# Kernel tuning notes

Measured on AMD Instinct MI355X. Metric: run time of the kernel, lower is better.

## Reference

```python
import jax, jax.numpy as jnp
import numpy as np

EPS_DIV = 1e-6    # safe_div clamp
EPS_NORM = 1e-12  # F.normalize eps
EPS_PD = 1e-6     # F.pairwise_distance eps (added to the difference)


def setup_inputs() -> dict:
    key = jax.random.key(0)
    k1, k2, k3 = jax.random.split(key, 3)
    B, N, D, C = 8, 2048, 512, 8192
    x = jax.random.normal(k1, (B, N, D), dtype=jnp.float32)
    W = jax.random.normal(k2, (D, D), dtype=jnp.float32) * (1.0 / np.sqrt(D))
    codebook = jax.random.normal(k3, (C, D), dtype=jnp.float32)
    return {"x": x, "W": W, "codebook": codebook}


def reference(x, W, codebook):
    sg = jax.lax.stop_gradient
    # implicit codebook = Linear(dim, dim, bias=False)(codebook)  -> codebook @ W^T
    imp = codebook @ W.T                                  # [C, D]

    lead = x.shape[:-1]
    D = x.shape[-1]
    xf = x.reshape(-1, D)                                 # [T, D]

    # nearest-neighbor search (no_grad in original): squared-dist argmin == cdist argmin
    d2 = (jnp.sum(xf * xf, axis=-1, keepdims=True)
          - 2.0 * (xf @ imp.T)
          + jnp.sum(imp * imp, axis=-1)[None, :])         # [T, C]
    indices = jnp.argmin(sg(d2), axis=-1)                 # [T]

    qf = imp[indices]                                     # [T, D] gather

    # commit loss: (pairwise_distance(x, q.detach())**2).mean(); torch adds eps to the diff
    diff = xf - sg(qf) + EPS_PD
    commit_loss = jnp.mean(jnp.sum(diff * diff, axis=-1))

    # rotation trick
    norm_x = jnp.linalg.norm(xf, axis=-1, keepdims=True)  # [T, 1]
    norm_q = jnp.linalg.norm(qf, axis=-1, keepdims=True)
    u = xf / jnp.maximum(norm_x, EPS_DIV)
    q = qf / jnp.maximum(norm_q, EPS_DIV)
    s = u + q
    w = sg(s / jnp.maximum(jnp.linalg.norm(s, axis=-1, keepdims=True), EPS_NORM))
    e = xf
    # e - 2 (e.w) w + 2 (e.u_sg) q_sg   (rank-1 products per row)
    rot = (e
           - 2.0 * jnp.sum(e * w, axis=-1, keepdims=True) * w
           + 2.0 * jnp.sum(e * sg(u), axis=-1, keepdims=True) * sg(q))
    quantized = rot * sg(norm_q / jnp.maximum(norm_x, EPS_DIV))

    quantized = quantized.reshape(*lead, D)
    indices = indices.reshape(*lead)
    return quantized, indices, commit_loss
```

## Files before the change

### kernel.cpp

```cpp
#include <hip/hip_runtime.h>
#include <cstdint>
#include <cstddef>

#define DD 512
#define TT 16384
#define CC 8192
#define SPLITC 64
#define EPS_DIV 1e-6f
#define EPS_NORM 1e-12f
#define EPS_PD 1e-6f

typedef _Float16 half8 __attribute__((ext_vector_type(8)));
typedef _Float16 half4 __attribute__((ext_vector_type(4)));
typedef float floatx4 __attribute__((ext_vector_type(4)));

#define GLDS16(g, l) __builtin_amdgcn_global_load_lds( \
    (const __attribute__((address_space(1))) void*)(g), \
    (__attribute__((address_space(3))) void*)(l), 16, 0, 0)

__global__ __launch_bounds__(128) void k_split(const float* __restrict__ src,
                                               _Float16* __restrict__ dst) {
  const int row = blockIdx.x;
  const int col = threadIdx.x * 4;
  float4 v = *(const float4*)(src + (size_t)row * DD + col);
  half4 h, l;
  h.x = (_Float16)v.x; l.x = (_Float16)(v.x - (float)h.x);
  h.y = (_Float16)v.y; l.y = (_Float16)(v.y - (float)h.y);
  h.z = (_Float16)v.z; l.z = (_Float16)(v.z - (float)h.z);
  h.w = (_Float16)v.w; l.w = (_Float16)(v.w - (float)h.w);
  *(half4*)(dst + (size_t)row * 1024 + col) = h;
  *(half4*)(dst + (size_t)row * 1024 + 512 + col) = l;
}

__global__ __launch_bounds__(128) void k_cast16(const float* __restrict__ src,
                                                _Float16* __restrict__ dst) {
  const int row = blockIdx.x;
  const int col = threadIdx.x * 4;
  float4 v = *(const float4*)(src + (size_t)row * DD + col);
  half4 h;
  h.x = (_Float16)v.x; h.y = (_Float16)v.y;
  h.z = (_Float16)v.z; h.w = (_Float16)v.w;
  *(half4*)(dst + (size_t)row * DD + col) = h;
}

__global__ __launch_bounds__(256) void k_gemm_mfma(
    const _Float16* __restrict__ cbs, const _Float16* __restrict__ Ws,
    float* __restrict__ imp, _Float16* __restrict__ ih) {
  __shared__ __align__(16) char smem[65536];
  const int tid = threadIdx.x;
  const int w = tid >> 6, lane = tid & 63;
  const int quad = lane >> 4, l15 = lane & 15;
  const int wm = (w & 1) * 64, wn = (w >> 1) * 64;
  const int c0 = blockIdx.x * 128;
  const int n0 = blockIdx.y * 128;

  const int srow8 = lane >> 3;
  const int scol = ((lane & 7) ^ srow8) << 3;
  size_t arow[4], brow[4];
#pragma unroll
  for (int j = 0; j < 4; ++j) {
    arow[j] = (size_t)(c0 + j * 32 + w * 8 + srow8) * 1024 + scol;
    brow[j] = (size_t)(n0 + j * 32 + w * 8 + srow8) * 1024 + scol;
  }
  int aoff[4], boff[4];
#pragma unroll
  for (int i = 0; i < 4; ++i) {
    aoff[i] = ((wm + i * 16 + l15) * 64 + ((quad ^ (l15 & 7)) << 3)) * 2;
    boff[i] = ((wn + i * 16 + l15) * 64 + ((quad ^ (l15 & 7)) << 3)) * 2;
  }

  auto stage = [&](int buf, int ak, int bk) {
    char* ab = smem + buf * 32768;
    char* bb = ab + 16384;
#pragma unroll
    for (int j = 0; j < 4; ++j) {
      GLDS16(cbs + arow[j] + ak, (_Float16*)ab + (j * 32 + w * 8) * 64);
      GLDS16(Ws  + brow[j] + bk, (_Float16*)bb + (j * 32 + w * 8) * 64);
    }
  };

  floatx4 acc[4][4] = {};
  stage(0, 0, 0);
#pragma unroll 2
  for (int it = 0; it < 24; ++it) {
    __syncthreads();
    if (it < 23) {
      const int n = it + 1;
      const int p = n >> 3, kk = n & 7;
      const int ak = ((p == 2) ? 512 : 0) + kk * 64;
      const int bk = ((p == 1) ? 512 : 0) + kk * 64;
      stage(n & 1, ak, bk);
    }
    const char* ab = smem + (it & 1) * 32768;
    const char* bb = ab + 16384;
#pragma unroll
    for (int ks = 0; ks < 2; ++ks) {
      const int kx = ks * 64;
      half8 a[4], b[4];
#pragma unroll
      for (int mi = 0; mi < 4; ++mi)
        a[mi] = *(const half8*)(ab + (aoff[mi] ^ kx));
#pragma unroll
      for (int ni = 0; ni < 4; ++ni)
        b[ni] = *(const half8*)(bb + (boff[ni] ^ kx));
#pragma unroll
      for (int mi = 0; mi < 4; ++mi)
#pragma unroll
        for (int ni = 0; ni < 4; ++ni)
          acc[mi][ni] = __builtin_amdgcn_mfma_f32_16x16x32_f16(
              a[mi], b[ni], acc[mi][ni], 0, 0, 0);
    }
  }
#pragma unroll
  for (int mi = 0; mi < 4; ++mi)
#pragma unroll
    for (int r = 0; r < 4; ++r) {
      const int c = c0 + wm + mi * 16 + quad * 4 + r;
#pragma unroll
      for (int ni = 0; ni < 4; ++ni) {
        const int d = n0 + wn + ni * 16 + l15;
        const float v = acc[mi][ni][r];
        imp[(size_t)c * DD + d] = v;
        ih[(size_t)c * DD + d] = (_Float16)v;
      }
    }
}

__global__ __launch_bounds__(256) void k_row_norm2(
    const float* __restrict__ imp, float* __restrict__ cnorm) {
  const int lane = threadIdx.x & 63;
  const int row = blockIdx.x * 4 + (threadIdx.x >> 6);
  const float* p = imp + (size_t)row * DD + lane * 8;
  float4 a = *(const float4*)p;
  float4 b = *(const float4*)(p + 4);
  float s = a.x * a.x + a.y * a.y + a.z * a.z + a.w * a.w +
            b.x * b.x + b.y * b.y + b.z * b.z + b.w * b.w;
#pragma unroll
  for (int m = 1; m < 64; m <<= 1) s += __shfl_xor(s, m);
  if (lane == 0) cnorm[row] = s;
}

__global__ __launch_bounds__(256) void k_dist_top2(
    const _Float16* __restrict__ xh, const _Float16* __restrict__ ih,
    const float* __restrict__ cnorm,
    float* __restrict__ bval, int* __restrict__ bidx) {
  __shared__ __align__(16) char smem[65536];
  const int tid = threadIdx.x;
  const int w = tid >> 6, lane = tid & 63;
  const int quad = lane >> 4, l15 = lane & 15;
  const int wm = (w & 1) * 64, wn = (w >> 1) * 64;
  const int r0 = blockIdx.x * 128;
  const int c0 = blockIdx.y * 128;

  const int srow8 = lane >> 3;
  const int scol = ((lane & 7) ^ srow8) << 3;
  size_t arow[4], brow[4];
#pragma unroll
  for (int j = 0; j < 4; ++j) {
    arow[j] = (size_t)(r0 + j * 32 + w * 8 + srow8) * DD + scol;
    brow[j] = (size_t)(c0 + j * 32 + w * 8 + srow8) * DD + scol;
  }
  int aoff[4], boff[4];
#pragma unroll
  for (int i = 0; i < 4; ++i) {
    aoff[i] = ((wm + i * 16 + l15) * 64 + ((quad ^ (l15 & 7)) << 3)) * 2;
    boff[i] = ((wn + i * 16 + l15) * 64 + ((quad ^ (l15 & 7)) << 3)) * 2;
  }

  auto stage = [&](int buf, int k0) {
    char* ab = smem + buf * 32768;
    char* bb = ab + 16384;
#pragma unroll
    for (int j = 0; j < 4; ++j) {
      GLDS16(xh + arow[j] + k0, (_Float16*)ab + (j * 32 + w * 8) * 64);
      GLDS16(ih + brow[j] + k0, (_Float16*)bb + (j * 32 + w * 8) * 64);
    }
  };

  floatx4 acc[4][4] = {};
  stage(0, 0);
#pragma unroll
  for (int kk = 0; kk < 8; ++kk) {
    __syncthreads();
    if (kk < 7) stage((kk + 1) & 1, (kk + 1) * 64);
    const char* ab = smem + (kk & 1) * 32768;
    const char* bb = ab + 16384;
#pragma unroll
    for (int ks = 0; ks < 2; ++ks) {
      const int kx = ks * 64;
      half8 a[4], b[4];
#pragma unroll
      for (int mi = 0; mi < 4; ++mi)
        a[mi] = *(const half8*)(ab + (aoff[mi] ^ kx));
#pragma unroll
      for (int ni = 0; ni < 4; ++ni)
        b[ni] = *(const half8*)(bb + (boff[ni] ^ kx));
#pragma unroll
      for (int mi = 0; mi < 4; ++mi)
#pragma unroll
        for (int ni = 0; ni < 4; ++ni)
          acc[mi][ni] = __builtin_amdgcn_mfma_f32_16x16x32_f16(
              a[mi], b[ni], acc[mi][ni], 0, 0, 0);
    }
  }
  float best[16];
  int bsti[16];
#pragma unroll
  for (int mi = 0; mi < 4; ++mi)
#pragma unroll
    for (int r = 0; r < 4; ++r) {
      const int s = mi * 4 + r;
      best[s] = 3.4e38f; bsti[s] = 0;
#pragma unroll
      for (int ni = 0; ni < 4; ++ni) {
        const int c = c0 + wn + ni * 16 + l15;
        const float v = fmaf(-2.0f, acc[mi][ni][r], cnorm[c]);
        if (v < best[s]) { best[s] = v; bsti[s] = c; }
      }
    }
  __syncthreads();
  float* rv = (float*)smem;
  int* ri = (int*)(smem + 16896);
  const int e = (w >> 1) * 16 + l15;
#pragma unroll
  for (int mi = 0; mi < 4; ++mi)
#pragma unroll
    for (int r = 0; r < 4; ++r) {
      const int row = wm + mi * 16 + quad * 4 + r;
      rv[row * 33 + e] = best[mi * 4 + r];
      ri[row * 33 + e] = bsti[mi * 4 + r];
    }
  __syncthreads();
  if (tid < 128) {
    float v1 = 3.4e38f, v2 = 3.4e38f;
    int i1 = 0x7fffffff, i2 = 0x7fffffff;
#pragma unroll
    for (int t = 0; t < 32; ++t) {
      const float v = rv[tid * 33 + t];
      const int i = ri[tid * 33 + t];
      if (v < v1 || (v == v1 && i < i1)) {
        v2 = v1; i2 = i1; v1 = v; i1 = i;
      } else if (v < v2 || (v == v2 && i < i2)) {
        v2 = v; i2 = i;
      }
    }
    const size_t o = ((size_t)blockIdx.y * TT + r0 + tid) * 2;
    bval[o] = v1; bval[o + 1] = v2;
    bidx[o] = i1; bidx[o + 1] = i2;
  }
}

__global__ __launch_bounds__(256) void k_epilogue(
    const float* __restrict__ x, const float* __restrict__ imp,
    const float* __restrict__ cnorm,
    const float* __restrict__ bval, const int* __restrict__ bidx,
    float* __restrict__ outq, float* __restrict__ outidx,
    float* __restrict__ rloss) {
  const int lane = threadIdx.x & 63;
  const int row = blockIdx.x * 4 + (threadIdx.x >> 6);
  const size_t o = ((size_t)lane * TT + row) * 2;
  float v1 = bval[o], v2 = bval[o + 1];
  int i1 = bidx[o], i2 = bidx[o + 1];
#pragma unroll
  for (int m = 1; m < 64; m <<= 1) {
    const float w1 = __shfl_xor(v1, m), w2 = __shfl_xor(v2, m);
    const int j1 = __shfl_xor(i1, m), j2 = __shfl_xor(i2, m);
    if (w1 < v1 || (w1 == v1 && j1 < i1)) {
      if (v1 < w2 || (v1 == w2 && i1 < j2)) { v2 = v1; i2 = i1; }
      else { v2 = w2; i2 = j2; }
      v1 = w1; i1 = j1;
    } else {
      if (w1 < v2 || (w1 == v2 && j1 < i2)) { v2 = w1; i2 = j1; }
    }
  }
  const float* xr = x + (size_t)row * DD + lane * 8;
  float e[8], qa[8], qb[8];
  *(float4*)&e[0] = *(const float4*)xr;
  *(float4*)&e[4] = *(const float4*)(xr + 4);
  const float* q1p = imp + (size_t)i1 * DD + lane * 8;
  const float* q2p = imp + (size_t)i2 * DD + lane * 8;
  *(float4*)&qa[0] = *(const float4*)q1p;
  *(float4*)&qa[4] = *(const float4*)(q1p + 4);
  *(float4*)&qb[0] = *(const float4*)q2p;
  *(float4*)&qb[4] = *(const float4*)(q2p + 4);
  float d1 = 0.f, d2 = 0.f;
#pragma unroll
  for (int k = 0; k < 8; ++k) {
    d1 = fmaf(e[k], qa[k], d1);
    d2 = fmaf(e[k], qb[k], d2);
  }
#pragma unroll
  for (int m = 1; m < 64; m <<= 1) {
    d1 += __shfl_xor(d1, m);
    d2 += __shfl_xor(d2, m);
  }
  const float s1 = fmaf(-2.0f, d1, cnorm[i1]);
  const float s2 = fmaf(-2.0f, d2, cnorm[i2]);
  const bool use2 = (s2 < s1) || (s2 == s1 && i2 < i1);
  const int idx = use2 ? i2 : i1;
  float q[8];
#pragma unroll
  for (int k = 0; k < 8; ++k) q[k] = use2 ? qb[k] : qa[k];

  float xx = 0.f, qq = 0.f, xq = 0.f, cl = 0.f;
#pragma unroll
  for (int k = 0; k < 8; ++k) {
    xx = fmaf(e[k], e[k], xx);
    qq = fmaf(q[k], q[k], qq);
    xq = fmaf(e[k], q[k], xq);
    float d = e[k] - q[k] + EPS_PD;
    cl = fmaf(d, d, cl);
  }
#pragma unroll
  for (int m = 1; m < 64; m <<= 1) {
    xx += __shfl_xor(xx, m);
    qq += __shfl_xor(qq, m);
    xq += __shfl_xor(xq, m);
    cl += __shfl_xor(cl, m);
  }
  const float nx = sqrtf(xx), nq = sqrtf(qq);
  const float dx = fmaxf(nx, EPS_DIV), dq = fmaxf(nq, EPS_DIV);
  const float uu = xx / (dx * dx);
  const float qq2 = qq / (dq * dq);
  const float uq = xq / (dx * dq);
  const float ss = uu + qq2 + 2.0f * uq;
  const float dn = fmaxf(sqrtf(ss), EPS_NORM);
  const float es = xx / dx + xq / dq;
  const float a = 2.0f * es / (dn * dn);
  const float b = 2.0f * (xx / dx);
  const float scale = nq / dx;

  float ov[8];
#pragma unroll
  for (int k = 0; k < 8; ++k) {
    const float qp = q[k] / dq;
    const float sk = e[k] / dx + qp;
    ov[k] = (e[k] - a * sk + b * qp) * scale;
  }
  float* op = outq + (size_t)row * DD + lane * 8;
  *(float4*)op = *(const float4*)&ov[0];
  *(float4*)(op + 4) = *(const float4*)&ov[4];
  if (lane == 0) {
    outidx[row] = (float)idx;
    rloss[row] = cl;
  }
}

__global__ __launch_bounds__(256) void k_loss_final(
    const float* __restrict__ rloss, float* __restrict__ out) {
  __shared__ double red[256];
  const int tid = threadIdx.x;
  double s = 0.0;
  for (int i = tid; i < TT; i += 256) s += (double)rloss[i];
  red[tid] = s;
  __syncthreads();
  for (int st = 128; st > 0; st >>= 1) {
    if (tid < st) red[tid] += red[tid + st];
    __syncthreads();
  }
  if (tid == 0) out[0] = (float)(red[0] / (double)TT);
}

extern "C" void kernel_launch(void* const* d_in, const int* in_sizes, int n_in,
                              void* d_out, int out_size, void* d_ws, size_t ws_size,
                              hipStream_t stream) {
  const float* x  = (const float*)d_in[0];
  const float* W  = (const float*)d_in[1];
  const float* cb = (const float*)d_in[2];
  float* out = (float*)d_out;

  float* imp = (float*)d_ws;
  _Float16* ih = (_Float16*)(imp + (size_t)CC * DD);
  _Float16* cbs = ih + (size_t)CC * DD;
  _Float16* xh = cbs;
  _Float16* Ws = cbs + (size_t)CC * 1024;
  float* cnorm = (float*)(Ws + (size_t)DD * 1024);
  float* bval  = cnorm + CC;
  int*   bidx  = (int*)(bval + (size_t)SPLITC * TT * 2);
  float* rloss = (float*)(bidx + (size_t)SPLITC * TT * 2);

  float* out_q    = out;
  float* out_idx  = out + (size_t)TT * DD;
  float* out_loss = out_idx + TT;

  k_split<<<CC, 128, 0, stream>>>(cb, cbs);
  k_split<<<DD, 128, 0, stream>>>(W, Ws);
  k_gemm_mfma<<<dim3(CC / 128, DD / 128), 256, 0, stream>>>(cbs, Ws, imp, ih);
  k_row_norm2<<<CC / 4, 256, 0, stream>>>(imp, cnorm);
  k_cast16<<<TT, 128, 0, stream>>>(x, xh);
  k_dist_top2<<<dim3(TT / 128, SPLITC), 256, 0, stream>>>(xh, ih, cnorm, bval, bidx);
  k_epilogue<<<TT / 4, 256, 0, stream>>>(x, imp, cnorm, bval, bidx, out_q, out_idx, rloss);
  k_loss_final<<<1, 256, 0, stream>>>(rloss, out_loss);
}
```

Before: 353.5 us.

## Loop over codebook tiles per block, fuse prep kernels, stage GEMM stores

The distance kernel now has each block sweep four 128-wide codebook tiles with a running argmin. The split across codebook chunks drops from 64 to 16, so the partial top-2 buffer and the epilogue merge shrink. The K tile goes from 64 to 32 with a smaller LDS footprint, which may raise occupancy. Separate prep launches are fused into combined kernels (codebook/W split, x cast plus codebook norms), and the codebook GEMM writes its output through LDS for coalesced stores. Fewer blocks and a longer serial loop per block trade parallelism for less reduction traffic.

Measured after the change: 422.9 us. 1.2x slower.

```diff
diff --git a/kernel.cpp b/kernel.cpp
--- a/kernel.cpp
+++ b/kernel.cpp
@@ -5,7 +5,7 @@
 #define DD 512
 #define TT 16384
 #define CC 8192
-#define SPLITC 64
+#define SPLITC 16
 #define EPS_DIV 1e-6f
 #define EPS_NORM 1e-12f
 #define EPS_PD 1e-6f
@@ -18,10 +18,21 @@
     (const __attribute__((address_space(1))) void*)(g), \
     (__attribute__((address_space(3))) void*)(l), 16, 0, 0)
 
-__global__ __launch_bounds__(128) void k_split(const float* __restrict__ src,
-                                               _Float16* __restrict__ dst) {
-  const int row = blockIdx.x;
-  const int col = threadIdx.x * 4;
+__global__ __launch_bounds__(256) void k_prep(
+    const float* __restrict__ cb, const float* __restrict__ W,
+    _Float16* __restrict__ cbs, _Float16* __restrict__ Ws) {
+  const int b = blockIdx.x;
+  const float* src;
+  _Float16* dst;
+  int row;
+  if (b < CC / 2) {
+    row = b * 2 + (threadIdx.x >> 7);
+    src = cb; dst = cbs;
+  } else {
+    row = (b - CC / 2) * 2 + (threadIdx.x >> 7);
+    src = W; dst = Ws;
+  }
+  const int col = (threadIdx.x & 127) * 4;
   float4 v = *(const float4*)(src + (size_t)row * DD + col);
   half4 h, l;
   h.x = (_Float16)v.x; l.x = (_Float16)(v.x - (float)h.x);
@@ -30,17 +41,6 @@
   h.w = (_Float16)v.w; l.w = (_Float16)(v.w - (float)h.w);
   *(half4*)(dst + (size_t)row * 1024 + col) = h;
   *(half4*)(dst + (size_t)row * 1024 + 512 + col) = l;
-}
-
-__global__ __launch_bounds__(128) void k_cast16(const float* __restrict__ src,
-                                                _Float16* __restrict__ dst) {
-  const int row = blockIdx.x;
-  const int col = threadIdx.x * 4;
-  float4 v = *(const float4*)(src + (size_t)row * DD + col);
-  half4 h;
-  h.x = (_Float16)v.x; h.y = (_Float16)v.y;
-  h.z = (_Float16)v.z; h.w = (_Float16)v.w;
-  *(half4*)(dst + (size_t)row * DD + col) = h;
 }
 
 __global__ __launch_bounds__(256) void k_gemm_mfma(
@@ -111,90 +111,126 @@
               a[mi], b[ni], acc[mi][ni], 0, 0, 0);
     }
   }
+  __syncthreads();
+  float* Csh = (float*)smem;
 #pragma unroll
   for (int mi = 0; mi < 4; ++mi)
 #pragma unroll
     for (int r = 0; r < 4; ++r) {
-      const int c = c0 + wm + mi * 16 + quad * 4 + r;
+      const int row = wm + mi * 16 + quad * 4 + r;
+      const int key = (row & 7) << 2;
 #pragma unroll
       for (int ni = 0; ni < 4; ++ni) {
-        const int d = n0 + wn + ni * 16 + l15;
-        const float v = acc[mi][ni][r];
-        imp[(size_t)c * DD + d] = v;
-        ih[(size_t)c * DD + d] = (_Float16)v;
+        const int col = wn + ni * 16 + l15;
+        Csh[row * 128 + (col ^ key)] = acc[mi][ni][r];
       }
     }
-}
-
-__global__ __launch_bounds__(256) void k_row_norm2(
+  __syncthreads();
+#pragma unroll
+  for (int i = 0; i < 16; ++i) {
+    const int row = (tid >> 5) * 16 + i;
+    const int col = (tid & 31) * 4;
+    const int key = (row & 7) << 2;
+    const float4 v = *(const float4*)&Csh[row * 128 + (col ^ key)];
+    *(float4*)&imp[(size_t)(c0 + row) * DD + n0 + col] = v;
+    half4 h;
+    h.x = (_Float16)v.x; h.y = (_Float16)v.y;
+    h.z = (_Float16)v.z; h.w = (_Float16)v.w;
+    *(half4*)&ih[(size_t)(c0 + row) * DD + n0 + col] = h;
+  }
+}
+
+__global__ __launch_bounds__(256) void k_cast_cnorm(
+    const float* __restrict__ x, _Float16* __restrict__ xh,
     const float* __restrict__ imp, float* __restrict__ cnorm) {
-  const int lane = threadIdx.x & 63;
-  const int row = blockIdx.x * 4 + (threadIdx.x >> 6);
-  const float* p = imp + (size_t)row * DD + lane * 8;
-  float4 a = *(const float4*)p;
-  float4 b = *(const float4*)(p + 4);
-  float s = a.x * a.x + a.y * a.y + a.z * a.z + a.w * a.w +
-            b.x * b.x + b.y * b.y + b.z * b.z + b.w * b.w;
-#pragma unroll
-  for (int m = 1; m < 64; m <<= 1) s += __shfl_xor(s, m);
-  if (lane == 0) cnorm[row] = s;
+  const int b = blockIdx.x;
+  if (b < TT / 2) {
+    const size_t base = (size_t)b * 1024 + threadIdx.x * 4;
+    float4 v = *(const float4*)(x + base);
+    half4 h;
+    h.x = (_Float16)v.x; h.y = (_Float16)v.y;
+    h.z = (_Float16)v.z; h.w = (_Float16)v.w;
+    *(half4*)(xh + base) = h;
+  } else {
+    const int lane = threadIdx.x & 63;
+    const int row = (b - TT / 2) * 4 + (threadIdx.x >> 6);
+    const float* p = imp + (size_t)row * DD + lane * 8;
+    float4 a = *(const float4*)p;
+    float4 c = *(const float4*)(p + 4);
+    float s = a.x * a.x + a.y * a.y + a.z * a.z + a.w * a.w +
+              c.x * c.x + c.y * c.y + c.z * c.z + c.w * c.w;
+#pragma unroll
+    for (int m = 1; m < 64; m <<= 1) s += __shfl_xor(s, m);
+    if (lane == 0) cnorm[row] = s;
+  }
 }
 
 __global__ __launch_bounds__(256) void k_dist_top2(
     const _Float16* __restrict__ xh, const _Float16* __restrict__ ih,
     const float* __restrict__ cnorm,
     float* __restrict__ bval, int* __restrict__ bidx) {
-  __shared__ __align__(16) char smem[65536];
+  __shared__ __align__(16) char smem[33792];
   const int tid = threadIdx.x;
   const int w = tid >> 6, lane = tid & 63;
   const int quad = lane >> 4, l15 = lane & 15;
   const int wm = (w & 1) * 64, wn = (w >> 1) * 64;
   const int r0 = blockIdx.x * 128;
-  const int c0 = blockIdx.y * 128;
-
-  const int srow8 = lane >> 3;
-  const int scol = ((lane & 7) ^ srow8) << 3;
-  size_t arow[4], brow[4];
-#pragma unroll
-  for (int j = 0; j < 4; ++j) {
-    arow[j] = (size_t)(r0 + j * 32 + w * 8 + srow8) * DD + scol;
-    brow[j] = (size_t)(c0 + j * 32 + w * 8 + srow8) * DD + scol;
+  const int cb0 = blockIdx.y * 512;
+
+  const int srow = lane >> 2;
+  const int scol = (((lane & 3) ^ ((lane >> 3) & 3)) << 3);
+  size_t aoffg[2];
+  int browt[2], ldst[2];
+#pragma unroll
+  for (int j = 0; j < 2; ++j) {
+    aoffg[j] = (size_t)(r0 + w * 32 + j * 16 + srow) * DD + scol;
+    browt[j] = w * 32 + j * 16 + srow;
+    ldst[j] = (w * 32 + j * 16) * 32;
   }
   int aoff[4], boff[4];
 #pragma unroll
   for (int i = 0; i < 4; ++i) {
-    aoff[i] = ((wm + i * 16 + l15) * 64 + ((quad ^ (l15 & 7)) << 3)) * 2;
-    boff[i] = ((wn + i * 16 + l15) * 64 + ((quad ^ (l15 & 7)) << 3)) * 2;
-  }
-
-  auto stage = [&](int buf, int k0) {
-    char* ab = smem + buf * 32768;
-    char* bb = ab + 16384;
-#pragma unroll
-    for (int j = 0; j < 4; ++j) {
-      GLDS16(xh + arow[j] + k0, (_Float16*)ab + (j * 32 + w * 8) * 64);
-      GLDS16(ih + brow[j] + k0, (_Float16*)bb + (j * 32 + w * 8) * 64);
+    const int pb = quad ^ ((l15 >> 1) & 3);
+    aoff[i] = ((wm + i * 16 + l15) * 32 + (pb << 3)) * 2;
+    boff[i] = ((wn + i * 16 + l15) * 32 + (pb << 3)) * 2;
+  }
+
+  auto stage = [&](int g) {
+    const int buf = g & 1;
+    const int ct = g >> 4, kk = g & 15;
+    const int k0 = kk * 32;
+    _Float16* ab = (_Float16*)(smem + buf * 16384);
+    _Float16* bb = (_Float16*)(smem + buf * 16384 + 8192);
+    const _Float16* bsrc = ih + (size_t)(cb0 + ct * 128) * DD;
+#pragma unroll
+    for (int j = 0; j < 2; ++j) {
+      GLDS16(xh + aoffg[j] + k0, ab + ldst[j]);
+      GLDS16(bsrc + (size_t)browt[j] * DD + scol + k0, bb + ldst[j]);
     }
   };
 
+  float best[16];
+  int bsti[16];
+#pragma unroll
+  for (int i = 0; i < 16; ++i) { best[i] = 3.4e38f; bsti[i] = 0; }
   floatx4 acc[4][4] = {};
-  stage(0, 0);
-#pragma unroll
-  for (int kk = 0; kk < 8; ++kk) {
-    __syncthreads();
-    if (kk < 7) stage((kk + 1) & 1, (kk + 1) * 64);
-    const char* ab = smem + (kk & 1) * 32768;
-    const char* bb = ab + 16384;
-#pragma unroll
-    for (int ks = 0; ks < 2; ++ks) {
-      const int kx = ks * 64;
+
+  stage(0);
+  for (int ct = 0; ct < 4; ++ct) {
+#pragma unroll 4
+    for (int kk = 0; kk < 16; ++kk) {
+      const int g = ct * 16 + kk;
+      __syncthreads();
+      if (g < 63) stage(g + 1);
+      const char* ab = smem + (g & 1) * 16384;
+      const char* bb = ab + 8192;
       half8 a[4], b[4];
 #pragma unroll
       for (int mi = 0; mi < 4; ++mi)
-        a[mi] = *(const half8*)(ab + (aoff[mi] ^ kx));
+        a[mi] = *(const half8*)(ab + aoff[mi]);
 #pragma unroll
       for (int ni = 0; ni < 4; ++ni)
-        b[ni] = *(const half8*)(bb + (boff[ni] ^ kx));
+        b[ni] = *(const half8*)(bb + boff[ni]);
 #pragma unroll
       for (int mi = 0; mi < 4; ++mi)
 #pragma unroll
@@ -202,22 +238,25 @@
           acc[mi][ni] = __builtin_amdgcn_mfma_f32_16x16x32_f16(
               a[mi], b[ni], acc[mi][ni], 0, 0, 0);
     }
-  }
-  float best[16];
-  int bsti[16];
-#pragma unroll
-  for (int mi = 0; mi < 4; ++mi)
-#pragma unroll
-    for (int r = 0; r < 4; ++r) {
-      const int s = mi * 4 + r;
-      best[s] = 3.4e38f; bsti[s] = 0;
-#pragma unroll
-      for (int ni = 0; ni < 4; ++ni) {
-        const int c = c0 + wn + ni * 16 + l15;
-        const float v = fmaf(-2.0f, acc[mi][ni][r], cnorm[c]);
-        if (v < best[s]) { best[s] = v; bsti[s] = c; }
-      }
-    }
+    const int cb1 = cb0 + ct * 128;
+#pragma unroll
+    for (int ni = 0; ni < 4; ++ni) {
+      const int c = cb1 + wn + ni * 16 + l15;
+      const float nn = cnorm[c];
+#pragma unroll
+      for (int mi = 0; mi < 4; ++mi)
+#pragma unroll
+        for (int r = 0; r < 4; ++r) {
+          const float v = fmaf(-2.0f, acc[mi][ni][r], nn);
+          const int s = mi * 4 + r;
+          if (v < best[s]) { best[s] = v; bsti[s] = c; }
+          if (ni == 3) acc[mi][3][r] = 0.0f;
+        }
+      if (ni < 3)
+#pragma unroll
+        for (int mi = 0; mi < 4; ++mi) acc[mi][ni] = (floatx4){0.f, 0.f, 0.f, 0.f};
+    }
+  }
   __syncthreads();
   float* rv = (float*)smem;
   int* ri = (int*)(smem + 16896);
@@ -258,11 +297,11 @@
     float* __restrict__ rloss) {
   const int lane = threadIdx.x & 63;
   const int row = blockIdx.x * 4 + (threadIdx.x >> 6);
-  const size_t o = ((size_t)lane * TT + row) * 2;
-  float v1 = bval[o], v2 = bval[o + 1];
-  int i1 = bidx[o], i2 = bidx[o + 1];
-#pragma unroll
-  for (int m = 1; m < 64; m <<= 1) {
+  const size_t o = ((size_t)((lane >> 1) & 15) * TT + row) * 2 + (lane & 1);
+  float v1 = bval[o], v2 = 3.4e38f;
+  int i1 = bidx[o], i2 = 0x7fffffff;
+#pragma unroll
+  for (int m = 1; m < 32; m <<= 1) {
     const float w1 = __shfl_xor(v1, m), w2 = __shfl_xor(v2, m);
     const int j1 = __shfl_xor(i1, m), j2 = __shfl_xor(i2, m);
     if (w1 < v1 || (w1 == v1 && j1 < i1)) {
@@ -383,11 +422,9 @@
   float* out_idx  = out + (size_t)TT * DD;
   float* out_loss = out_idx + TT;
 
-  k_split<<<CC, 128, 0, stream>>>(cb, cbs);
-  k_split<<<DD, 128, 0, stream>>>(W, Ws);
+  k_prep<<<CC / 2 + DD / 2, 256, 0, stream>>>(cb, W, cbs, Ws);
   k_gemm_mfma<<<dim3(CC / 128, DD / 128), 256, 0, stream>>>(cbs, Ws, imp, ih);
-  k_row_norm2<<<CC / 4, 256, 0, stream>>>(imp, cnorm);
-  k_cast16<<<TT, 128, 0, stream>>>(x, xh);
+  k_cast_cnorm<<<TT / 2 + CC / 4, 256, 0, stream>>>(x, xh, imp, cnorm);
   k_dist_top2<<<dim3(TT / 128, SPLITC), 256, 0, stream>>>(xh, ih, cnorm, bval, bidx);
   k_epilogue<<<TT / 4, 256, 0, stream>>>(x, imp, cnorm, bval, bidx, out_q, out_idx, rloss);
   k_loss_final<<<1, 256, 0, stream>>>(rloss, out_loss);
```
